# Kernel optimization log

Hardware: AMD Instinct MI355X
Metric: run time of the kernel (lower is better)

Reference implementation:

```python
import jax, jax.numpy as jnp
import numpy as np


def _nearest_resize(x, Hl, Wl):
    # x: [B, Hf, Wf] -> [B, Hl, Wl], PyTorch F.interpolate(mode='nearest') semantics:
    # src_idx = floor(out_idx * in_size / out_size)
    B, Hf, Wf = x.shape
    ri = (jnp.arange(Hl) * Hf) // Hl
    ci = (jnp.arange(Wl) * Wf) // Wl
    return x[:, ri[:, None], ci[None, :]]


def _nearest_centroid(f, c):
    # f: [B, C, H, W], c: [K, C]
    # argmin_k ||f - c_k||_2 over channels == argmin of squared distance
    f2 = jnp.sum(f * f, axis=1)                       # [B, H, W]
    c2 = jnp.sum(c * c, axis=1)                       # [K]
    cross = jnp.einsum('bchw,kc->bkhw', f, c)         # [B, K, H, W]
    d2 = f2[:, None] - 2.0 * cross + c2[None, :, None, None]
    return jnp.argmin(d2, axis=1)                     # [B, H, W] int


def setup_inputs() -> dict:
    key = jax.random.key(0)
    k1, k2, k3, k4, k5, k6 = jax.random.split(key, 6)
    B, C, Hf, Wf = 4, 256, 64, 128
    K = 19  # class_num
    Hl, Wl = 512, 1024
    return {
        'feature_s2t': jax.random.normal(k1, (B, C, Hf, Wf), dtype=jnp.float32),
        'feature_target': jax.random.normal(k2, (B, C, Hf, Wf), dtype=jnp.float32),
        'label_s2t': jax.random.randint(k3, (B, Hl, Wl), 0, K, dtype=jnp.int64) if jax.config.jax_enable_x64 else jax.random.randint(k3, (B, Hl, Wl), 0, K, dtype=jnp.int32),
        'label_target': jax.random.randint(k4, (B, Hl, Wl), 0, K, dtype=jnp.int32),
        'centroid_s2t': jax.random.normal(k5, (K, C), dtype=jnp.float32),
        'centroid_target': jax.random.normal(k6, (K, C), dtype=jnp.float32),
    }


def reference(feature_s2t, feature_target, label_s2t, label_target, centroid_s2t, centroid_target):
    # feature_s2t is matched against the TARGET-domain centroids and vice versa
    # (cross assignment, exactly as in the torch forward).
    mask_s2t = _nearest_centroid(feature_s2t, centroid_target)     # [B, Hf, Wf]
    mask_target = _nearest_centroid(feature_target, centroid_s2t)  # [B, Hf, Wf]
    Hl, Wl = label_s2t.shape[1], label_s2t.shape[2]
    mask_s2t = _nearest_resize(mask_s2t, Hl, Wl).astype(jnp.int32)
    Hl2, Wl2 = label_target.shape[1], label_target.shape[2]
    mask_target = _nearest_resize(mask_target, Hl2, Wl2).astype(jnp.int32)
    return (mask_s2t, mask_target)
```

## Files before the change

kernel.cpp:

```cpp
#include <hip/hip_runtime.h>

#define K   19
#define C   256
#define HF  64
#define WF  128
#define HW  (HF * WF)
#define BB  4
#define HL  512
#define WL  1024

#define TAU 0.03f

#define CPAD 264
#define DPAD 66

typedef __attribute__((ext_vector_type(8)))  short bf16x8;
typedef __attribute__((ext_vector_type(16))) float f32x16;

__global__ __launch_bounds__(256, 4) void centroid_mask_kernel(
    const float* __restrict__ feat0,
    const float* __restrict__ feat1,
    const float* __restrict__ cent0,
    const float* __restrict__ cent1,
    int* __restrict__ out)
{
    __shared__ __align__(16) unsigned short chi[K * CPAD];
    __shared__ __align__(16) unsigned short clo[K * CPAD];
    __shared__ float  dbuf[2][2][16][DPAD];
    __shared__ double c2p[K][8];
    __shared__ double sc2d[K];
    __shared__ float  sc2f[K];

    const int map = blockIdx.y;
    const float* __restrict__ feat = (map == 0) ? feat0 : feat1;
    const float* __restrict__ cent = (map == 0) ? cent0 : cent1;

    const int tid  = threadIdx.x;
    const int lane = tid & 63;
    const int wv   = __builtin_amdgcn_readfirstlane(tid >> 6);

    for (int i = tid; i < K * C; i += 256) {
        const int k = i >> 8, c = i & (C - 1);
        const unsigned u = __float_as_uint(cent[i]);
        const float r = __uint_as_float(u) - __uint_as_float(u & 0xffff0000u);
        chi[k * CPAD + c] = (unsigned short)(u >> 16);
        clo[k * CPAD + c] = (unsigned short)(__float_as_uint(r) >> 16);
    }
    if (tid < K * 8) {
        const int k = tid >> 3, sl = tid & 7;
        const float* cp = cent + k * C + sl * 32;
        double s = 0.0;
        #pragma unroll
        for (int j = 0; j < 32; ++j) { double v = (double)cp[j]; s = fma(v, v, s); }
        c2p[k][sl] = s;
    }
    __syncthreads();
    if (tid < K) {
        double s = 0.0;
        #pragma unroll
        for (int j = 0; j < 8; ++j) s += c2p[tid][j];
        sc2d[tid] = s;
        sc2f[tid] = (float)s;
    }

    const int tile = wv >> 1, kh = wv & 1;
    const int hl2  = (lane >> 5) & 1;
    const int pp   = blockIdx.x * 64 + tile * 32 + (lane & 31);
    const int hw   = pp & (HW - 1);
    const int b    = pp >> 13;

    const float* __restrict__ fp = feat + (size_t)b * C * HW + hw;
    const int cb0  = kh * 128 + hl2 * 8;
    const int bidx = min(lane & 31, 18) * CPAD + kh * 128 + hl2 * 8;

    f32x16 acc;
    #pragma unroll
    for (int r = 0; r < 16; ++r) acc[r] = 0.f;

    #pragma unroll
    for (int s = 0; s < 8; ++s) {
        const int cb = cb0 + s * 16;
        float fv[8];
        #pragma unroll
        for (int j = 0; j < 8; ++j)
            fv[j] = fp[(size_t)(cb + j) * HW];

        union { unsigned u[4]; bf16x8 v; } ah, al, bh, bl;
        #pragma unroll
        for (int j = 0; j < 4; ++j) {
            const unsigned u0 = __float_as_uint(fv[2*j]);
            const unsigned u1 = __float_as_uint(fv[2*j+1]);
            ah.u[j] = (u0 >> 16) | (u1 & 0xffff0000u);
            const float r0 = fv[2*j]   - __uint_as_float(u0 & 0xffff0000u);
            const float r1 = fv[2*j+1] - __uint_as_float(u1 & 0xffff0000u);
            al.u[j] = (__float_as_uint(r0) >> 16)
                    | (__float_as_uint(r1) & 0xffff0000u);
        }
        bh.v = *(const bf16x8*)&chi[bidx + s * 16];
        bl.v = *(const bf16x8*)&clo[bidx + s * 16];

        acc = __builtin_amdgcn_mfma_f32_32x32x16_bf16(ah.v, bh.v, acc, 0, 0, 0);
        acc = __builtin_amdgcn_mfma_f32_32x32x16_bf16(ah.v, bl.v, acc, 0, 0, 0);
        acc = __builtin_amdgcn_mfma_f32_32x32x16_bf16(al.v, bh.v, acc, 0, 0, 0);
    }

    {
        float* dst = &dbuf[tile][kh][0][hl2 * 32 + (lane & 31)];
        #pragma unroll
        for (int r = 0; r < 16; ++r) dst[r * DPAD] = acc[r];
    }
    __syncthreads();

    if (tid < 64) {
        const int l   = tid;
        const int tl  = l >> 5, px = l & 31;
        const int h   = (px >> 2) & 1;
        const int reg = (px & 3) | ((px >> 3) << 2);
        const int bse = h * 32;

        const int ppx = blockIdx.x * 64 + l;
        const int phw = ppx & (HW - 1);
        const int pb  = ppx >> 13;

        float d[K];
        #pragma unroll
        for (int k = 0; k < K; ++k) {
            const float s = dbuf[tl][0][reg][bse + k] + dbuf[tl][1][reg][bse + k];
            d[k] = sc2f[k] - 2.0f * s;
        }
        int best = 0; float m1 = d[0];
        #pragma unroll
        for (int k = 1; k < K; ++k) if (d[k] < m1) { m1 = d[k]; best = k; }

        unsigned cmask = 0u;
        #pragma unroll
        for (int k = 0; k < K; ++k) if (d[k] - m1 < TAU) cmask |= (1u << k);

        const bool need = (cmask & (cmask - 1)) != 0u;
        unsigned long long ball = __ballot(need);
        while (ball) {
            const int sx = (int)__builtin_ctzll(ball);
            ball &= ball - 1;
            const unsigned pm  = __shfl(cmask, sx, 64);
            const int      fhw = __shfl(phw,   sx, 64);
            const int      fb  = __shfl(pb,    sx, 64);
            const float* __restrict__ fcol = feat + (size_t)fb * C * HW + fhw;

            const int c0 = tid << 2;
            double pf[4];
            #pragma unroll
            for (int j = 0; j < 4; ++j)
                pf[j] = (double)fcol[(size_t)(c0 + j) * HW];

            double bd = 1e300; int bi = 0;
            unsigned mm = pm;
            while (mm) {
                const int k = (int)__builtin_ctz(mm);
                mm &= mm - 1;
                const float* __restrict__ ck = cent + (size_t)k * C + c0;
                double s = 0.0;
                #pragma unroll
                for (int j = 0; j < 4; ++j)
                    s = fma(pf[j], (double)ck[j], s);
                #pragma unroll
                for (int off = 1; off < 64; off <<= 1)
                    s += __shfl_xor(s, off, 64);
                const double dk = sc2d[k] - 2.0 * s;
                if (dk < bd) { bd = dk; bi = k; }
            }
            if (tid == sx) best = bi;
        }

        const int w = phw & (WF - 1);
        const int hh = phw >> 7;
        int4 v = make_int4(best, best, best, best);
        int* __restrict__ ob = out + (size_t)map * (BB * HL * WL)
                                   + (size_t)pb * (HL * WL)
                                   + (size_t)(hh * 8) * WL + (size_t)(w * 8);
        #pragma unroll
        for (int r = 0; r < 8; ++r) {
            *(int4*)(ob + (size_t)r * WL)     = v;
            *(int4*)(ob + (size_t)r * WL + 4) = v;
        }
    }
}

extern "C" void kernel_launch(void* const* d_in, const int* in_sizes, int n_in,
                              void* d_out, int out_size, void* d_ws, size_t ws_size,
                              hipStream_t stream) {
    const float* feature_s2t     = (const float*)d_in[0];
    const float* feature_target  = (const float*)d_in[1];
    const float* centroid_s2t    = (const float*)d_in[4];
    const float* centroid_target = (const float*)d_in[5];
    int* out = (int*)d_out;

    dim3 grid(32768 / 64, 2);
    dim3 block(256);
    hipLaunchKernelGGL(centroid_mask_kernel, grid, block, 0, stream,
                       feature_s2t, feature_target,
                       centroid_target, centroid_s2t, out);
}
```

Measured before the change: 22.72 us.

## Split channel reduction across four waves per 32-pixel tile and alias LDS

Each block now covers 32 pixels instead of 64, and its four waves each reduce a quarter of the channels (64) rather than two waves per tile reducing half. Grid size doubles to spread work across more blocks. The distance buffer now aliases the centroid split arrays in a shared LDS pool, separated by an extra barrier, so LDS per block drops and the launch-bounds occupancy hint rises from 4 to 6. The costs are that each block re-converts the centroids for only half as many pixels, the epilogue reduction and fix-up use only half a wave, and each block pays an extra barrier.

```diff
diff --git a/kernel.cpp b/kernel.cpp
--- a/kernel.cpp
+++ b/kernel.cpp
@@ -13,23 +13,27 @@
 
 #define CPAD 264
 #define DPAD 66
+#define CHI_BYTES (K * CPAD * 2)
+#define POOL_BYTES (2 * CHI_BYTES)
 
 typedef __attribute__((ext_vector_type(8)))  short bf16x8;
 typedef __attribute__((ext_vector_type(16))) float f32x16;
 
-__global__ __launch_bounds__(256, 4) void centroid_mask_kernel(
+__global__ __launch_bounds__(256, 6) void centroid_mask_kernel(
     const float* __restrict__ feat0,
     const float* __restrict__ feat1,
     const float* __restrict__ cent0,
     const float* __restrict__ cent1,
     int* __restrict__ out)
 {
-    __shared__ __align__(16) unsigned short chi[K * CPAD];
-    __shared__ __align__(16) unsigned short clo[K * CPAD];
-    __shared__ float  dbuf[2][2][16][DPAD];
+    __shared__ __align__(16) unsigned char pool[POOL_BYTES];
     __shared__ double c2p[K][8];
     __shared__ double sc2d[K];
     __shared__ float  sc2f[K];
+
+    unsigned short* __restrict__ chi = (unsigned short*)pool;
+    unsigned short* __restrict__ clo = (unsigned short*)(pool + CHI_BYTES);
+    float*          __restrict__ dbf = (float*)pool;
 
     const int map = blockIdx.y;
     const float* __restrict__ feat = (map == 0) ? feat0 : feat1;
@@ -63,22 +67,22 @@
         sc2f[tid] = (float)s;
     }
 
-    const int tile = wv >> 1, kh = wv & 1;
+    const int kh   = wv;
     const int hl2  = (lane >> 5) & 1;
-    const int pp   = blockIdx.x * 64 + tile * 32 + (lane & 31);
+    const int pp   = blockIdx.x * 32 + (lane & 31);
     const int hw   = pp & (HW - 1);
     const int b    = pp >> 13;
 
     const float* __restrict__ fp = feat + (size_t)b * C * HW + hw;
-    const int cb0  = kh * 128 + hl2 * 8;
-    const int bidx = min(lane & 31, 18) * CPAD + kh * 128 + hl2 * 8;
+    const int cb0  = kh * 64 + hl2 * 8;
+    const int bidx = min(lane & 31, 18) * CPAD + kh * 64 + hl2 * 8;
 
     f32x16 acc;
     #pragma unroll
     for (int r = 0; r < 16; ++r) acc[r] = 0.f;
 
     #pragma unroll
-    for (int s = 0; s < 8; ++s) {
+    for (int s = 0; s < 4; ++s) {
         const int cb = cb0 + s * 16;
         float fv[8];
         #pragma unroll
@@ -104,28 +108,32 @@
         acc = __builtin_amdgcn_mfma_f32_32x32x16_bf16(al.v, bh.v, acc, 0, 0, 0);
     }
 
+    __syncthreads();
+
     {
-        float* dst = &dbuf[tile][kh][0][hl2 * 32 + (lane & 31)];
+        float* dst = &dbf[(kh * 16) * DPAD + hl2 * 32 + (lane & 31)];
         #pragma unroll
         for (int r = 0; r < 16; ++r) dst[r * DPAD] = acc[r];
     }
     __syncthreads();
 
     if (tid < 64) {
-        const int l   = tid;
-        const int tl  = l >> 5, px = l & 31;
+        const int px  = lane & 31;
         const int h   = (px >> 2) & 1;
         const int reg = (px & 3) | ((px >> 3) << 2);
         const int bse = h * 32;
 
-        const int ppx = blockIdx.x * 64 + l;
+        const int ppx = blockIdx.x * 32 + px;
         const int phw = ppx & (HW - 1);
         const int pb  = ppx >> 13;
 
         float d[K];
         #pragma unroll
         for (int k = 0; k < K; ++k) {
-            const float s = dbuf[tl][0][reg][bse + k] + dbuf[tl][1][reg][bse + k];
+            const float s = (dbf[(0 * 16 + reg) * DPAD + bse + k]
+                           + dbf[(1 * 16 + reg) * DPAD + bse + k])
+                          + (dbf[(2 * 16 + reg) * DPAD + bse + k]
+                           + dbf[(3 * 16 + reg) * DPAD + bse + k]);
             d[k] = sc2f[k] - 2.0f * s;
         }
         int best = 0; float m1 = d[0];
@@ -137,7 +145,7 @@
         for (int k = 0; k < K; ++k) if (d[k] - m1 < TAU) cmask |= (1u << k);
 
         const bool need = (cmask & (cmask - 1)) != 0u;
-        unsigned long long ball = __ballot(need);
+        unsigned long long ball = __ballot(need && (lane < 32));
         while (ball) {
             const int sx = (int)__builtin_ctzll(ball);
             ball &= ball - 1;
@@ -146,7 +154,7 @@
             const int      fb  = __shfl(pb,    sx, 64);
             const float* __restrict__ fcol = feat + (size_t)fb * C * HW + fhw;
 
-            const int c0 = tid << 2;
+            const int c0 = lane << 2;
             double pf[4];
             #pragma unroll
             for (int j = 0; j < 4; ++j)
@@ -168,19 +176,21 @@
                 const double dk = sc2d[k] - 2.0 * s;
                 if (dk < bd) { bd = dk; bi = k; }
             }
-            if (tid == sx) best = bi;
-        }
-
-        const int w = phw & (WF - 1);
-        const int hh = phw >> 7;
-        int4 v = make_int4(best, best, best, best);
-        int* __restrict__ ob = out + (size_t)map * (BB * HL * WL)
-                                   + (size_t)pb * (HL * WL)
-                                   + (size_t)(hh * 8) * WL + (size_t)(w * 8);
-        #pragma unroll
-        for (int r = 0; r < 8; ++r) {
-            *(int4*)(ob + (size_t)r * WL)     = v;
-            *(int4*)(ob + (size_t)r * WL + 4) = v;
+            if (lane == sx) best = bi;
+        }
+
+        if (lane < 32) {
+            const int w  = phw & (WF - 1);
+            const int hh = phw >> 7;
+            int4 v = make_int4(best, best, best, best);
+            int* __restrict__ ob = out + (size_t)map * (BB * HL * WL)
+                                       + (size_t)pb * (HL * WL)
+                                       + (size_t)(hh * 8) * WL + (size_t)(w * 8);
+            #pragma unroll
+            for (int r = 0; r < 8; ++r) {
+                *(int4*)(ob + (size_t)r * WL)     = v;
+                *(int4*)(ob + (size_t)r * WL + 4) = v;
+            }
         }
     }
 }
@@ -194,7 +204,7 @@
     const float* centroid_target = (const float*)d_in[5];
     int* out = (int*)d_out;
 
-    dim3 grid(32768 / 64, 2);
+    dim3 grid(32768 / 32, 2);
     dim3 block(256);
     hipLaunchKernelGGL(centroid_mask_kernel, grid, block, 0, stream,
                        feature_s2t, feature_target,
```

Measured after the change: 24.12 us. 1.06x slower.

## Split channel reduction across four waves per tile with 512-thread blocks

Applied to the files above, without the earlier changes.

Doubles the block to 512 threads so each 32-pixel tile's 256-channel reduction is split across four waves instead of two, halving the per-wave MFMA chain and feature loads. The partial-sum buffer now aliases the centroid shared arrays through a pooled LDS allocation guarded by an extra barrier, and the load loop is software-pipelined with two register buffers. The aim is more memory-level parallelism and latency hiding. The cost is an extra barrier, a four-way partial-sum combine, and higher per-block LDS and register pressure that may limit occupancy.

```diff
diff --git a/kernel.cpp b/kernel.cpp
--- a/kernel.cpp
+++ b/kernel.cpp
@@ -13,24 +13,29 @@
 
 #define CPAD 264
 #define DPAD 66
+#define CHI_BYTES  (K * CPAD * 2)
+#define DBUF_BYTES (8 * 16 * DPAD * 4)
+#define POOL_BYTES 33792
 
 typedef __attribute__((ext_vector_type(8)))  short bf16x8;
 typedef __attribute__((ext_vector_type(16))) float f32x16;
 
-__global__ __launch_bounds__(256, 4) void centroid_mask_kernel(
+__global__ __launch_bounds__(512, 8) void centroid_mask_kernel(
     const float* __restrict__ feat0,
     const float* __restrict__ feat1,
     const float* __restrict__ cent0,
     const float* __restrict__ cent1,
     int* __restrict__ out)
 {
-    __shared__ __align__(16) unsigned short chi[K * CPAD];
-    __shared__ __align__(16) unsigned short clo[K * CPAD];
-    __shared__ float  dbuf[2][2][16][DPAD];
+    __shared__ __align__(16) unsigned char pool[POOL_BYTES];
     __shared__ double c2p[K][8];
     __shared__ double sc2d[K];
     __shared__ float  sc2f[K];
 
+    unsigned short* __restrict__ chi = (unsigned short*)pool;
+    unsigned short* __restrict__ clo = (unsigned short*)(pool + CHI_BYTES);
+    float*          __restrict__ dbf = (float*)pool;
+
     const int map = blockIdx.y;
     const float* __restrict__ feat = (map == 0) ? feat0 : feat1;
     const float* __restrict__ cent = (map == 0) ? cent0 : cent1;
@@ -38,8 +43,10 @@
     const int tid  = threadIdx.x;
     const int lane = tid & 63;
     const int wv   = __builtin_amdgcn_readfirstlane(tid >> 6);
-
-    for (int i = tid; i < K * C; i += 256) {
+    const int tile = wv >> 2;
+    const int khq  = wv & 3;
+
+    for (int i = tid; i < K * C; i += 512) {
         const int k = i >> 8, c = i & (C - 1);
         const unsigned u = __float_as_uint(cent[i]);
         const float r = __uint_as_float(u) - __uint_as_float(u & 0xffff0000u);
@@ -63,49 +70,61 @@
         sc2f[tid] = (float)s;
     }
 
-    const int tile = wv >> 1, kh = wv & 1;
     const int hl2  = (lane >> 5) & 1;
     const int pp   = blockIdx.x * 64 + tile * 32 + (lane & 31);
     const int hw   = pp & (HW - 1);
     const int b    = pp >> 13;
 
     const float* __restrict__ fp = feat + (size_t)b * C * HW + hw;
-    const int cb0  = kh * 128 + hl2 * 8;
-    const int bidx = min(lane & 31, 18) * CPAD + kh * 128 + hl2 * 8;
+    const int cb0  = khq * 64 + hl2 * 8;
+    const int bidx = min(lane & 31, 18) * CPAD + khq * 64 + hl2 * 8;
 
     f32x16 acc;
     #pragma unroll
     for (int r = 0; r < 16; ++r) acc[r] = 0.f;
 
-    #pragma unroll
-    for (int s = 0; s < 8; ++s) {
-        const int cb = cb0 + s * 16;
-        float fv[8];
-        #pragma unroll
-        for (int j = 0; j < 8; ++j)
-            fv[j] = fp[(size_t)(cb + j) * HW];
-
-        union { unsigned u[4]; bf16x8 v; } ah, al, bh, bl;
-        #pragma unroll
-        for (int j = 0; j < 4; ++j) {
-            const unsigned u0 = __float_as_uint(fv[2*j]);
-            const unsigned u1 = __float_as_uint(fv[2*j+1]);
-            ah.u[j] = (u0 >> 16) | (u1 & 0xffff0000u);
-            const float r0 = fv[2*j]   - __uint_as_float(u0 & 0xffff0000u);
-            const float r1 = fv[2*j+1] - __uint_as_float(u1 & 0xffff0000u);
-            al.u[j] = (__float_as_uint(r0) >> 16)
-                    | (__float_as_uint(r1) & 0xffff0000u);
-        }
-        bh.v = *(const bf16x8*)&chi[bidx + s * 16];
-        bl.v = *(const bf16x8*)&clo[bidx + s * 16];
-
-        acc = __builtin_amdgcn_mfma_f32_32x32x16_bf16(ah.v, bh.v, acc, 0, 0, 0);
-        acc = __builtin_amdgcn_mfma_f32_32x32x16_bf16(ah.v, bl.v, acc, 0, 0, 0);
-        acc = __builtin_amdgcn_mfma_f32_32x32x16_bf16(al.v, bh.v, acc, 0, 0, 0);
-    }
+    float fvA[8], fvB[8];
+
+#define LOADS(buf, s)                                                   \
+    {                                                                   \
+        _Pragma("unroll")                                               \
+        for (int j = 0; j < 8; ++j)                                     \
+            buf[j] = fp[(size_t)(cb0 + (s) * 16 + j) * HW];             \
+    }
+#define STEP(buf, s)                                                    \
+    {                                                                   \
+        union { unsigned u[4]; bf16x8 v; } ah, al, bh, bl;              \
+        _Pragma("unroll")                                               \
+        for (int j = 0; j < 4; ++j) {                                   \
+            const unsigned u0 = __float_as_uint(buf[2*j]);              \
+            const unsigned u1 = __float_as_uint(buf[2*j+1]);            \
+            ah.u[j] = (u0 >> 16) | (u1 & 0xffff0000u);                  \
+            const float r0 = buf[2*j]   - __uint_as_float(u0 & 0xffff0000u); \
+            const float r1 = buf[2*j+1] - __uint_as_float(u1 & 0xffff0000u); \
+            al.u[j] = (__float_as_uint(r0) >> 16)                       \
+                    | (__float_as_uint(r1) & 0xffff0000u);              \
+        }                                                               \
+        bh.v = *(const bf16x8*)&chi[bidx + (s) * 16];                   \
+        bl.v = *(const bf16x8*)&clo[bidx + (s) * 16];                   \
+        acc = __builtin_amdgcn_mfma_f32_32x32x16_bf16(ah.v, bh.v, acc, 0, 0, 0); \
+        acc = __builtin_amdgcn_mfma_f32_32x32x16_bf16(ah.v, bl.v, acc, 0, 0, 0); \
+        acc = __builtin_amdgcn_mfma_f32_32x32x16_bf16(al.v, bh.v, acc, 0, 0, 0); \
+    }
+
+    LOADS(fvA, 0)
+    LOADS(fvB, 1)
+    STEP(fvA, 0) LOADS(fvA, 2)
+    STEP(fvB, 1) LOADS(fvB, 3)
+    STEP(fvA, 2)
+    STEP(fvB, 3)
+
+#undef LOADS
+#undef STEP
+
+    __syncthreads();
 
     {
-        float* dst = &dbuf[tile][kh][0][hl2 * 32 + (lane & 31)];
+        float* dst = &dbf[((tile * 4 + khq) * 16) * DPAD + hl2 * 32 + (lane & 31)];
         #pragma unroll
         for (int r = 0; r < 16; ++r) dst[r * DPAD] = acc[r];
     }
@@ -125,7 +144,10 @@
         float d[K];
         #pragma unroll
         for (int k = 0; k < K; ++k) {
-            const float s = dbuf[tl][0][reg][bse + k] + dbuf[tl][1][reg][bse + k];
+            const float s = (dbf[((tl*4+0)*16 + reg) * DPAD + bse + k]
+                           + dbf[((tl*4+1)*16 + reg) * DPAD + bse + k])
+                          + (dbf[((tl*4+2)*16 + reg) * DPAD + bse + k]
+                           + dbf[((tl*4+3)*16 + reg) * DPAD + bse + k]);
             d[k] = sc2f[k] - 2.0f * s;
         }
         int best = 0; float m1 = d[0];
@@ -171,7 +193,7 @@
             if (tid == sx) best = bi;
         }
 
-        const int w = phw & (WF - 1);
+        const int w  = phw & (WF - 1);
         const int hh = phw >> 7;
         int4 v = make_int4(best, best, best, best);
         int* __restrict__ ob = out + (size_t)map * (BB * HL * WL)
@@ -195,7 +217,7 @@
     int* out = (int*)d_out;
 
     dim3 grid(32768 / 64, 2);
-    dim3 block(256);
+    dim3 block(512);
     hipLaunchKernelGGL(centroid_mask_kernel, grid, block, 0, stream,
                        feature_s2t, feature_target,
                        centroid_target, centroid_s2t, out);
```

New measurement: 24.48 us. 7.8% more time.
